# Kernel tuning notes

Hardware: AMD Instinct MI355X
Metric: run time of the kernel (lower is better)

The kernel has to match this reference:

```python
import jax, jax.numpy as jnp
import numpy as np

B, S, D = 2, 2048, 2048
H, KV, HD = 32, 8, 64          # n_heads, n_kv_heads, head_dim
REP = H // KV                  # 4
THETA = 10000.0


def _rotate_half(u):
    h = u.shape[-1] // 2
    return jnp.concatenate([-u[..., h:], u[..., :h]], axis=-1)


def setup_inputs() -> dict:
    key = jax.random.key(0)
    ks = jax.random.split(key, 5)
    x = jax.random.normal(ks[0], (B, S, D), dtype=jnp.float32)
    Wq = jax.random.normal(ks[1], (D, H * HD), dtype=jnp.float32) * 0.02
    Wk = jax.random.normal(ks[2], (D, KV * HD), dtype=jnp.float32) * 0.02
    Wv = jax.random.normal(ks[3], (D, KV * HD), dtype=jnp.float32) * 0.02
    Wo = jax.random.normal(ks[4], (H * HD, D), dtype=jnp.float32) * 0.02
    return {"x": x, "Wq": Wq, "Wk": Wk, "Wv": Wv, "Wo": Wo}


def reference(x, Wq, Wk, Wv, Wo):
    b, s, d = x.shape
    # QKV projections (nn.Linear, no bias)
    q = (x @ Wq).reshape(b, s, H, HD).transpose(0, 2, 1, 3)   # [B,H,S,HD]
    k = (x @ Wk).reshape(b, s, KV, HD).transpose(0, 2, 1, 3)  # [B,KV,S,HD]
    v = (x @ Wv).reshape(b, s, KV, HD).transpose(0, 2, 1, 3)  # [B,KV,S,HD]

    # RoPE (position_offset = 0)
    inv_freq = 1.0 / (THETA ** (jnp.arange(0, HD, 2, dtype=jnp.float32) / HD))
    freqs = jnp.outer(jnp.arange(s, dtype=jnp.float32), inv_freq)  # [S,HD/2]
    emb = jnp.concatenate([freqs, freqs], axis=-1)                  # [S,HD]
    cos, sin = jnp.cos(emb), jnp.sin(emb)
    q = q * cos + _rotate_half(q) * sin
    k = k * cos + _rotate_half(k) * sin

    # Grouped attention: avoid materializing repeated KV tensors.
    qg = q.reshape(b, KV, REP, s, HD)                               # [B,KV,REP,S,HD]
    scale = 1.0 / np.sqrt(HD)
    scores = jnp.einsum('bgrqd,bgkd->bgrqk', qg, k) * scale         # [B,KV,REP,S,S]
    causal = jnp.tril(jnp.ones((s, s), dtype=bool))
    scores = jnp.where(causal, scores, jnp.finfo(jnp.float32).min)
    probs = jax.nn.softmax(scores.astype(jnp.float32), axis=-1).astype(q.dtype)
    out = jnp.einsum('bgrqk,bgkd->bgrqd', probs, v)                 # [B,KV,REP,S,HD]
    out = out.reshape(b, H, s, HD).transpose(0, 2, 1, 3).reshape(b, s, H * HD)
    return out @ Wo                                                  # [B,S,D]
```

## Files before the change

### kernel.cpp

```cpp
#include <hip/hip_runtime.h>
#include <math.h>

typedef __bf16 bf16_t;
typedef bf16_t bf16x8 __attribute__((ext_vector_type(8)));
typedef bf16_t bf16x4 __attribute__((ext_vector_type(4)));
typedef float floatx4 __attribute__((ext_vector_type(4)));
typedef short short4v __attribute__((ext_vector_type(4)));

#define MFMA16(a, b, c) __builtin_amdgcn_mfma_f32_16x16x32_bf16((a), (b), (c), 0, 0, 0)

#if __has_builtin(__builtin_amdgcn_exp2f)
#define PEXP(x) __builtin_amdgcn_exp2f(x)
#define SCORE_SCALE (0.125f * 1.4426950408889634f)
#else
#define PEXP(x) __expf(x)
#define SCORE_SCALE 0.125f
#endif

#if __has_builtin(__builtin_amdgcn_mfma_f32_16x16x16bf16_1k)
#define HAVE_MFMA_K16 1
__device__ __forceinline__ floatx4 mfma_k16(bf16x4 a, bf16x4 b, floatx4 c)
{
    union { bf16x4 v; short4v s; } ua, ub;
    ua.v = a; ub.v = b;
    return __builtin_amdgcn_mfma_f32_16x16x16bf16_1k(ua.s, ub.s, c, 0, 0, 0);
}
#endif

union PU { unsigned u[2]; bf16x4 v; };
union BU { unsigned u[4]; bf16x8 v; };

__device__ __forceinline__ void gld16(const void* g, void* lds)
{
    __builtin_amdgcn_global_load_lds(
        reinterpret_cast<const __attribute__((address_space(1))) void*>(
            reinterpret_cast<uintptr_t>(g)),
        reinterpret_cast<__attribute__((address_space(3))) void*>(
            (unsigned int)reinterpret_cast<uintptr_t>(lds)),
        16, 0, 0);
}

template <int RND>
__device__ __forceinline__ void stageT(
    const bf16_t* __restrict__ g, int K, int r0, int k0,
    bf16_t* lds, int tid, int wave)
{
    #pragma unroll
    for (int i = 0; i < RND; ++i) {
        int c = i * 512 + tid, r = c >> 3, s = c & 7;
        gld16(g + (size_t)(r0 + r) * K + k0 + ((s ^ (r & 7)) << 3),
              lds + (size_t)(i * 512 + wave * 64) * 8);
    }
}

template <typename TC, int BN>
__device__ __forceinline__ void gemm256_body(
    const bf16_t* __restrict__ A, const bf16_t* __restrict__ Bt,
    TC* __restrict__ C, int row0, int col0, int N, int K, bf16_t* smem)
{
    constexpr int NT = BN / 64;
    constexpr int NH = NT / 2;
    constexpr int RB = BN / 64;

    const int tid  = threadIdx.x;
    const int wave = tid >> 6, lane = tid & 63;
    const int quad = lane >> 4, l16 = lane & 15;
    const int wm = (wave >> 2) * 128;
    const int wn = (wave & 3) * (BN / 4);

    bf16_t* As0 = smem;
    bf16_t* As1 = smem + 256 * 64;
    bf16_t* Bs0 = smem + 2 * 256 * 64;
    bf16_t* Bs1 = Bs0 + BN * 64;

    const int ntile = K >> 6;

    floatx4 acc[8][NT] = {};

    stageT<4>(A, K, row0, 0, As0, tid, wave);
    stageT<RB>(Bt, K, col0, 0, Bs0, tid, wave);
    stageT<4>(A, K, row0, 64, As1, tid, wave);

    #pragma unroll 1
    for (int u = 0; u < ntile; ++u) {
        const int d = u & 1;
        bf16_t* Asd = d ? As1 : As0;
        bf16_t* Bsd = d ? Bs1 : Bs0;

        if (u + 1 < ntile)
            __asm__ volatile("s_waitcnt vmcnt(4)" ::: "memory");
        else
            __asm__ volatile("s_waitcnt vmcnt(0)" ::: "memory");
        __builtin_amdgcn_s_barrier();
        __asm__ volatile("" ::: "memory");

        if (u + 1 < ntile)
            stageT<RB>(Bt, K, col0, (u + 1) << 6, d ? Bs0 : Bs1, tid, wave);

        bf16x8 af[8][2], bfr[NH][2];
        #pragma unroll
        for (int mt = 0; mt < 8; ++mt)
            #pragma unroll
            for (int kh = 0; kh < 2; ++kh) {
                int ar = wm + mt * 16 + l16;
                af[mt][kh] = *(const bf16x8*)&Asd[ar * 64 +
                    (((kh * 4 + quad) ^ (ar & 7)) << 3)];
            }
        #pragma unroll
        for (int j = 0; j < NH; ++j)
            #pragma unroll
            for (int kh = 0; kh < 2; ++kh) {
                int br = wn + j * 16 + l16;
                bfr[j][kh] = *(const bf16x8*)&Bsd[br * 64 +
                    (((kh * 4 + quad) ^ (br & 7)) << 3)];
            }

        __builtin_amdgcn_s_setprio(1);
        #pragma unroll
        for (int kh = 0; kh < 2; ++kh)
            #pragma unroll
            for (int mt = 0; mt < 8; ++mt)
                #pragma unroll
                for (int j = 0; j < NH; ++j)
                    acc[mt][j] = MFMA16(af[mt][kh], bfr[j][kh], acc[mt][j]);
        __builtin_amdgcn_s_setprio(0);

        __asm__ volatile("s_waitcnt lgkmcnt(0)" ::: "memory");
        __builtin_amdgcn_s_barrier();
        __asm__ volatile("" ::: "memory");

        if (u + 2 < ntile)
            stageT<4>(A, K, row0, (u + 2) << 6, Asd, tid, wave);

        bf16x8 bf1[NH][2];
        #pragma unroll
        for (int j = 0; j < NH; ++j)
            #pragma unroll
            for (int kh = 0; kh < 2; ++kh) {
                int br = wn + (NH + j) * 16 + l16;
                bf1[j][kh] = *(const bf16x8*)&Bsd[br * 64 +
                    (((kh * 4 + quad) ^ (br & 7)) << 3)];
            }

        __builtin_amdgcn_s_setprio(1);
        #pragma unroll
        for (int kh = 0; kh < 2; ++kh)
            #pragma unroll
            for (int mt = 0; mt < 8; ++mt)
                #pragma unroll
                for (int j = 0; j < NH; ++j)
                    acc[mt][NH + j] = MFMA16(af[mt][kh], bf1[j][kh],
                                             acc[mt][NH + j]);
        __builtin_amdgcn_s_setprio(0);
    }

    #pragma unroll
    for (int mt = 0; mt < 8; ++mt)
        #pragma unroll
        for (int nt = 0; nt < NT; ++nt)
            #pragma unroll
            for (int r = 0; r < 4; ++r)
                C[(size_t)(row0 + wm + mt * 16 + quad * 4 + r) * N
                  + col0 + wn + nt * 16 + l16] = (TC)acc[mt][nt][r];
}

__global__ __launch_bounds__(512, 2) void gemm256_qkv(
    const bf16_t* __restrict__ A, const bf16_t* __restrict__ BtQ,
    const bf16_t* __restrict__ BtK, const bf16_t* __restrict__ BtV,
    bf16_t* __restrict__ CQ, bf16_t* __restrict__ CK, bf16_t* __restrict__ CV)
{
    extern __shared__ __align__(16) bf16_t smem[];
    const int x = blockIdx.x;
    const bf16_t* Bt; bf16_t* C; int N, col0;
    if (x < 8)       { Bt = BtQ; C = CQ; N = 2048; col0 = x * 256; }
    else if (x < 10) { Bt = BtK; C = CK; N = 512;  col0 = (x - 8) * 256; }
    else             { Bt = BtV; C = CV; N = 512;  col0 = (x - 10) * 256; }
    gemm256_body<bf16_t, 256>(A, Bt, C, blockIdx.y * 256, col0, N, 2048, smem);
}

__global__ __launch_bounds__(512, 2) void gemm256_out(
    const bf16_t* __restrict__ A, const bf16_t* __restrict__ Bt,
    float* __restrict__ C)
{
    extern __shared__ __align__(16) bf16_t smem[];
    gemm256_body<float, 128>(A, Bt, C, blockIdx.y * 256, blockIdx.x * 128,
                             2048, 2048, smem);
}

__device__ __forceinline__ void transpose_body(
    const float* __restrict__ W, bf16_t* __restrict__ Wt, int K, int N,
    int bx, int by, float (*t)[33], int tid)
{
    int tx = tid & 31, ty = tid >> 5;
    #pragma unroll
    for (int i = 0; i < 32; i += 8)
        t[ty + i][tx] = W[(size_t)(by + ty + i) * N + bx + tx];
    __syncthreads();
    #pragma unroll
    for (int i = 0; i < 32; i += 8)
        Wt[(size_t)(bx + ty + i) * K + by + tx] = (bf16_t)t[tx][ty + i];
}

__global__ __launch_bounds__(256) void prep_all(
    const float* __restrict__ x, const float* __restrict__ Wq,
    const float* __restrict__ Wk, const float* __restrict__ Wv,
    bf16_t* __restrict__ xb, bf16_t* __restrict__ WqT,
    bf16_t* __restrict__ WkT, bf16_t* __restrict__ WvT)
{
    __shared__ float t[32][33];
    const int blk = blockIdx.x, tid = threadIdx.x;
    if (blk < 8192) {
        int i = blk * 256 + tid;
        float4 f = ((const float4*)x)[i];
        bf16x4 v = {(bf16_t)f.x, (bf16_t)f.y, (bf16_t)f.z, (bf16_t)f.w};
        ((bf16x4*)xb)[i] = v;
    } else if (blk < 12288) {
        int r = blk - 8192;
        transpose_body(Wq, WqT, 2048, 2048, (r & 63) * 32, (r >> 6) * 32, t, tid);
    } else if (blk < 13312) {
        int r = blk - 12288;
        transpose_body(Wk, WkT, 2048, 512, (r & 15) * 32, (r >> 4) * 32, t, tid);
    } else {
        int r = blk - 13312;
        transpose_body(Wv, WvT, 2048, 512, (r & 15) * 32, (r >> 4) * 32, t, tid);
    }
}

__global__ __launch_bounds__(256) void mid_all(
    bf16_t* __restrict__ Kw, const bf16_t* __restrict__ Vw,
    bf16_t* __restrict__ VtG, const float* __restrict__ Wo,
    bf16_t* __restrict__ WoT)
{
    __shared__ float tf[32][33];
    __shared__ bf16_t tb[32][34];
    const int blk = blockIdx.x, tid = threadIdx.x;
    if (blk < 4096) {
        int idx = blk * 256 + tid;
        int i   = idx & 31;
        int h   = (idx >> 5) & 7;
        int row = idx >> 8;
        int pos = row & 2047;
        float invf = powf(10000.0f, -(float)i / 32.0f);
        float sv, cv;
        sincosf((float)pos * invf, &sv, &cv);
        size_t base = (size_t)row * 512 + (size_t)h * 64 + i;
        float a  = (float)Kw[base];
        float b2 = (float)Kw[base + 32];
        Kw[base]      = (bf16_t)(a * cv - b2 * sv);
        Kw[base + 32] = (bf16_t)(b2 * cv + a * sv);
    } else if (blk < 6144) {
        int r  = blk - 4096;
        int bz = r >> 10, r2 = r & 1023;
        int bx = (r2 & 15) * 32, by = (r2 >> 4) * 32;
        int tx = tid & 31, ty = tid >> 5;
        #pragma unroll
        for (int i = 0; i < 32; i += 8)
            tb[ty + i][tx] = Vw[((size_t)bz * 2048 + by + ty + i) * 512 + bx + tx];
        __syncthreads();
        #pragma unroll
        for (int i = 0; i < 32; i += 8)
            VtG[((size_t)bz * 512 + bx + ty + i) * 2048 + by + tx] = tb[tx][ty + i];
    } else {
        int r = blk - 6144;
        transpose_body(Wo, WoT, 2048, 2048, (r & 63) * 32, (r >> 6) * 32, tf, tid);
    }
}

__global__ __launch_bounds__(256, 2) void gqa_attn(
    const bf16_t* __restrict__ Q, const bf16_t* __restrict__ Kc,
    const bf16_t* __restrict__ Vt, bf16_t* __restrict__ AO)
{
    __shared__ alignas(16) bf16_t Ks[2][128 * 64];
    __shared__ alignas(16) bf16_t Vs[2][128 * 64];

    const int bid = blockIdx.x;
    const int l   = (bid & 7) * 64 + (bid >> 3);
    const int g   = l >> 6;
    const int b   = (l >> 5) & 1;
    const int x   = l & 31;

    const int tid  = threadIdx.x;
    const int wave = tid >> 6, lane = tid & 63;
    const int quad = lane >> 4, l16 = lane & 15;
    const int h = g * 4 + wave;

    #pragma unroll 1
    for (int t = 0; t < 2; ++t) {
        const int qt = t ? x : (63 - x);
        const int q0 = qt * 32;
        int qb[2];
        qb[0] = q0;
        qb[1] = q0 + 16;

        bf16x8 qf[2][2];
        #pragma unroll
        for (int mt = 0; mt < 2; ++mt) {
            int qrow = qb[mt] + l16;
            const bf16_t* qp = Q + (size_t)(b * 2048 + qrow) * 2048 + h * 64 + quad * 8;
            bf16x8 lo = *(const bf16x8*)qp;
            bf16x8 hi = *(const bf16x8*)(qp + 32);
            #pragma unroll
            for (int j = 0; j < 8; ++j) {
                int d = quad * 8 + j;
                float invf = powf(10000.0f, -(float)d / 32.0f);
                float sv, cv;
                sincosf((float)qrow * invf, &sv, &cv);
                float a = (float)lo[j], c2 = (float)hi[j];
                qf[mt][0][j] = (bf16_t)((a * cv - c2 * sv) * SCORE_SCALE);
                qf[mt][1][j] = (bf16_t)((c2 * cv + a * sv) * SCORE_SCALE);
            }
        }

        floatx4 o[2][4] = {};
        floatx4 ls4[2] = {};

        const int ktmax = qt >> 1;
        const int nwin  = (ktmax >> 1) + 1;

        auto STAGE = [&](int win, int dst) {
            const int kbase = win * 128;
            #pragma unroll
            for (int i = 0; i < 4; ++i) {
                int c = i * 256 + tid, r = c >> 3, s = c & 7;
                int sw = (s ^ (r & 7)) << 3;
                gld16(Kc + (size_t)(b * 2048 + kbase + r) * 512 + g * 64 + sw,
                      &Ks[dst][(i * 256 + wave * 64) * 8]);
            }
            #pragma unroll
            for (int i = 0; i < 4; ++i) {
                int c = i * 256 + tid;
                int ci = c & 511, hw = c >> 9;
                int r = ci >> 3, s = ci & 7;
                int sw = (s ^ (r & 7)) << 3;
                gld16(Vt + (size_t)(b * 512 + g * 64 + r) * 2048
                         + kbase + hw * 64 + sw,
                      &Vs[dst][(i * 256 + wave * 64) * 8]);
            }
        };

        __asm__ volatile("s_waitcnt lgkmcnt(0)" ::: "memory");
        __builtin_amdgcn_s_barrier();
        STAGE(0, 0);

        #pragma unroll 1
        for (int win = 0; win < nwin; ++win) {
            const int cur = win & 1;
            if (win + 1 < nwin) {
                STAGE(win + 1, cur ^ 1);
                __asm__ volatile("s_waitcnt vmcnt(8)" ::: "memory");
            } else {
                __asm__ volatile("s_waitcnt vmcnt(0)" ::: "memory");
            }
            __builtin_amdgcn_s_barrier();

            #pragma unroll
            for (int hw = 0; hw < 2; ++hw) {
                const int kt = 2 * win + hw;
                if (kt <= ktmax) {
                    const bf16_t* Ksh = &Ks[cur][hw * 4096];
                    const bf16_t* Vsh = &Vs[cur][hw * 4096];

                    floatx4 st[2][4] = {};
                    __builtin_amdgcn_s_setprio(1);
                    #pragma unroll
                    for (int nt = 0; nt < 4; ++nt) {
                        int kr = nt * 16 + l16;
                        bf16x8 kf0 = *(const bf16x8*)&Ksh[kr * 64 + ((quad ^ (kr & 7)) << 3)];
                        bf16x8 kf1 = *(const bf16x8*)&Ksh[kr * 64 + (((4 + quad) ^ (kr & 7)) << 3)];
                        st[0][nt] = MFMA16(kf0, qf[0][0], st[0][nt]);
                        st[0][nt] = MFMA16(kf1, qf[0][1], st[0][nt]);
                        st[1][nt] = MFMA16(kf0, qf[1][0], st[1][nt]);
                        st[1][nt] = MFMA16(kf1, qf[1][1], st[1][nt]);
                    }
                    __builtin_amdgcn_s_setprio(0);

                    PU pk[2][4];
                    const bool diag = (kt == ktmax);
                    #pragma unroll
                    for (int mt = 0; mt < 2; ++mt) {
                        const int qa = qb[mt] + l16;
                        #pragma unroll
                        for (int nt = 0; nt < 4; ++nt) {
                            float pv[4];
                            #pragma unroll
                            for (int r = 0; r < 4; ++r) {
                                float e = PEXP(st[mt][nt][r]);
                                if (diag) {
                                    int ka = kt * 64 + nt * 16 + quad * 4 + r;
                                    if (ka > qa) e = 0.f;
                                }
                                ls4[mt][r] += e;
                                pv[r] = e;
                            }
                            pk[mt][nt].v = bf16x4{(bf16_t)pv[0], (bf16_t)pv[1],
                                                  (bf16_t)pv[2], (bf16_t)pv[3]};
                        }
                    }

#ifdef HAVE_MFMA_K16
                    __builtin_amdgcn_s_setprio(1);
                    #pragma unroll
                    for (int nt = 0; nt < 4; ++nt)
                        #pragma unroll
                        for (int dt = 0; dt < 4; ++dt) {
                            int vr = dt * 16 + l16;
                            int slot = ((nt << 1) | (quad >> 1)) ^ (vr & 7);
                            bf16x4 va = *(const bf16x4*)&Vsh[vr * 64 + (slot << 3)
                                                             + ((quad & 1) << 2)];
                            o[0][dt] = mfma_k16(va, pk[0][nt].v, o[0][dt]);
                            o[1][dt] = mfma_k16(va, pk[1][nt].v, o[1][dt]);
                        }
                    __builtin_amdgcn_s_setprio(0);
#else
                    #pragma unroll
                    for (int H = 0; H < 2; ++H) {
                        BU bfv[2];
                        #pragma unroll
                        for (int mt = 0; mt < 2; ++mt) {
                            #pragma unroll
                            for (int j = 0; j < 4; ++j) {
                                int srcl = (((quad & 1) << 1) + (j >> 1)) * 16 + l16;
                                unsigned a0 = (unsigned)__shfl((int)pk[mt][2 * H].u[j & 1], srcl, 64);
                                unsigned a1 = (unsigned)__shfl((int)pk[mt][2 * H + 1].u[j & 1], srcl, 64);
                                bfv[mt].u[j] = (quad >> 1) ? a1 : a0;
                            }
                        }
                        #pragma unroll
                        for (int dt = 0; dt < 4; ++dt) {
                            int vr = dt * 16 + l16;
                            bf16x8 va = *(const bf16x8*)&Vsh[vr * 64
                                          + ((((H << 2) | quad) ^ (vr & 7)) << 3)];
                            o[0][dt] = MFMA16(va, bfv[0].v, o[0][dt]);
                            o[1][dt] = MFMA16(va, bfv[1].v, o[1][dt]);
                        }
                    }
#endif
                }
            }

            __asm__ volatile("s_waitcnt lgkmcnt(0)" ::: "memory");
            __builtin_amdgcn_s_barrier();
        }

        #pragma unroll
        for (int mt = 0; mt < 2; ++mt) {
            float l2 = ls4[mt][0] + ls4[mt][1] + ls4[mt][2] + ls4[mt][3];
            l2 += __shfl_xor(l2, 16, 64);
            l2 += __shfl_xor(l2, 32, 64);
            float rc = 1.0f / l2;
            #pragma unroll
            for (int dt = 0; dt < 4; ++dt) {
                bf16x4 ov = {(bf16_t)(o[mt][dt][0] * rc), (bf16_t)(o[mt][dt][1] * rc),
                             (bf16_t)(o[mt][dt][2] * rc), (bf16_t)(o[mt][dt][3] * rc)};
                *(bf16x4*)&AO[(size_t)(b * 2048 + qb[mt] + l16) * 2048
                              + h * 64 + dt * 16 + quad * 4] = ov;
            }
        }
    }
}

extern "C" void kernel_launch(void* const* d_in, const int* in_sizes, int n_in,
                              void* d_out, int out_size, void* d_ws, size_t ws_size,
                              hipStream_t stream)
{
    const float* x  = (const float*)d_in[0];
    const float* Wq = (const float*)d_in[1];
    const float* Wk = (const float*)d_in[2];
    const float* Wv = (const float*)d_in[3];
    const float* Wo = (const float*)d_in[4];
    float* out = (float*)d_out;

    const size_t MB = 1024 * 1024;
    char* ws = (char*)d_ws;
    bf16_t* xb_AO = (bf16_t*)(ws);
    bf16_t* WqoT  = (bf16_t*)(ws + 16 * MB);
    bf16_t* WkT   = (bf16_t*)(ws + 24 * MB);
    bf16_t* WvT   = (bf16_t*)(ws + 26 * MB);
    bf16_t* Qw    = (bf16_t*)(ws + 28 * MB);
    bf16_t* Kw    = (bf16_t*)(ws + 44 * MB);
    bf16_t* Vw    = (bf16_t*)(ws + 48 * MB);
    bf16_t* VtG   = (bf16_t*)(ws + 52 * MB);

    static bool s_attr = false;
    if (!s_attr) {
        hipFuncSetAttribute(reinterpret_cast<const void*>(gemm256_qkv),
                            hipFuncAttributeMaxDynamicSharedMemorySize, 131072);
        hipFuncSetAttribute(reinterpret_cast<const void*>(gemm256_out),
                            hipFuncAttributeMaxDynamicSharedMemorySize, 98304);
        s_attr = true;
    }

    prep_all<<<14336, 256, 0, stream>>>(x, Wq, Wk, Wv, xb_AO, WqoT, WkT, WvT);

    gemm256_qkv<<<dim3(12, 16), 512, 131072, stream>>>(
        xb_AO, WqoT, WkT, WvT, Qw, Kw, Vw);

    mid_all<<<10240, 256, 0, stream>>>(Kw, Vw, VtG, Wo, WqoT);

    gqa_attn<<<dim3(512), 256, 0, stream>>>(Qw, Kw, VtG, xb_AO);

    gemm256_out<<<dim3(16, 16), 512, 98304, stream>>>(xb_AO, WqoT, out);
}
```

Measured before the change: 290.9 us.

## Restructure GEMM main loop into four-phase ping-pong schedule with split staging

Rewrites the shared 256-row GEMM body used by the QKV and output projections as a four-phase loop. Each phase reads a quarter of the A/B fragments from LDS, issues part of the next tile's global-to-LDS staging, then runs a barrier-bracketed MFMA block. The aim is finer interleaving of memory traffic and matrix math and lower register pressure by holding only half the A fragments at a time. In exchange each K-tile now has eight barriers instead of two and must re-read B fragments from LDS.

```diff
diff --git a/kernel.cpp b/kernel.cpp
--- a/kernel.cpp
+++ b/kernel.cpp
@@ -40,27 +40,32 @@
         16, 0, 0);
 }
 
-template <int RND>
-__device__ __forceinline__ void stageT(
-    const bf16_t* __restrict__ g, int K, int r0, int k0,
-    bf16_t* lds, int tid, int wave)
-{
-    #pragma unroll
-    for (int i = 0; i < RND; ++i) {
-        int c = i * 512 + tid, r = c >> 3, s = c & 7;
-        gld16(g + (size_t)(r0 + r) * K + k0 + ((s ^ (r & 7)) << 3),
-              lds + (size_t)(i * 512 + wave * 64) * 8);
-    }
+template <int N>
+__device__ __forceinline__ void vmw()
+{
+    __asm__ volatile("s_waitcnt vmcnt(%0)" :: "n"(N) : "memory");
+}
+
+__device__ __forceinline__ void barx()
+{
+    __asm__ volatile("" ::: "memory");
+    __builtin_amdgcn_s_barrier();
+    __asm__ volatile("" ::: "memory");
+}
+
+__device__ __forceinline__ void lgk0()
+{
+    __asm__ volatile("s_waitcnt lgkmcnt(0)" ::: "memory");
 }
 
 template <typename TC, int BN>
-__device__ __forceinline__ void gemm256_body(
+__device__ __forceinline__ void gemm_ph_body(
     const bf16_t* __restrict__ A, const bf16_t* __restrict__ Bt,
     TC* __restrict__ C, int row0, int col0, int N, int K, bf16_t* smem)
 {
-    constexpr int NT = BN / 64;
-    constexpr int NH = NT / 2;
-    constexpr int RB = BN / 64;
+    constexpr int NT  = BN / 64;
+    constexpr int NH  = NT / 2;
+    constexpr int RBH = BN / 128;
 
     const int tid  = threadIdx.x;
     const int wave = tid >> 6, lane = tid & 63;
@@ -76,83 +81,112 @@
     const int ntile = K >> 6;
 
     floatx4 acc[8][NT] = {};
-
-    stageT<4>(A, K, row0, 0, As0, tid, wave);
-    stageT<RB>(Bt, K, col0, 0, Bs0, tid, wave);
-    stageT<4>(A, K, row0, 64, As1, tid, wave);
+    bf16x8  af[4][2];
+    bf16x8  bfr[NH][2];
+    bf16x8  bf1[NH][2];
+
+#define PH_STG_A(Bf, h, uu) do {                                              \
+    _Pragma("unroll")                                                         \
+    for (int _i = 0; _i < 2; ++_i) {                                          \
+        int _c = _i * 512 + tid, _r = (h) * 128 + (_c >> 3), _s = _c & 7;     \
+        gld16(A + (size_t)(row0 + _r) * K + ((uu) << 6)                       \
+                + ((_s ^ (_r & 7)) << 3),                                     \
+              (Bf) + (h) * 8192 + (_i * 512 + wave * 64) * 8);                \
+    } } while (0)
+
+#define PH_STG_B(Bf, h, uu) do {                                              \
+    _Pragma("unroll")                                                         \
+    for (int _i = 0; _i < RBH; ++_i) {                                        \
+        int _c = _i * 512 + tid, _r = (h) * (BN / 2) + (_c >> 3), _s = _c & 7;\
+        gld16(Bt + (size_t)(col0 + _r) * K + ((uu) << 6)                      \
+                 + ((_s ^ (_r & 7)) << 3),                                    \
+              (Bf) + (h) * (BN / 2) * 64 + (_i * 512 + wave * 64) * 8);       \
+    } } while (0)
+
+#define PH_RD_A(MH) do {                                                      \
+    _Pragma("unroll")                                                         \
+    for (int _i = 0; _i < 4; ++_i)                                            \
+        _Pragma("unroll")                                                     \
+        for (int _kh = 0; _kh < 2; ++_kh) {                                   \
+            int _ar = wm + ((MH) * 4 + _i) * 16 + l16;                        \
+            af[_i][_kh] = *(const bf16x8*)&Asd[_ar * 64 +                     \
+                (((_kh * 4 + quad) ^ (_ar & 7)) << 3)];                       \
+        } } while (0)
+
+#define PH_RD_B(Reg, NF) do {                                                 \
+    _Pragma("unroll")                                                         \
+    for (int _j = 0; _j < NH; ++_j)                                           \
+        _Pragma("unroll")                                                     \
+        for (int _kh = 0; _kh < 2; ++_kh) {                                   \
+            int _br = wn + ((NF) * NH + _j) * 16 + l16;                       \
+            Reg[_j][_kh] = *(const bf16x8*)&Bsd[_br * 64 +                    \
+                (((_kh * 4 + quad) ^ (_br & 7)) << 3)];                       \
+        } } while (0)
+
+#define PH_MM(MB, Reg, NF) do {                                               \
+    __builtin_amdgcn_s_setprio(1);                                            \
+    _Pragma("unroll")                                                         \
+    for (int _kh = 0; _kh < 2; ++_kh)                                         \
+        _Pragma("unroll")                                                     \
+        for (int _i = 0; _i < 4; ++_i)                                        \
+            _Pragma("unroll")                                                 \
+            for (int _j = 0; _j < NH; ++_j)                                   \
+                acc[(MB) * 4 + _i][(NF) * NH + _j] =                          \
+                    MFMA16(af[_i][_kh], Reg[_j][_kh],                         \
+                           acc[(MB) * 4 + _i][(NF) * NH + _j]);               \
+    __builtin_amdgcn_s_setprio(0);                                            \
+} while (0)
+
+    PH_STG_A(As0, 0, 0); PH_STG_A(As0, 1, 0);
+    PH_STG_B(Bs0, 0, 0); PH_STG_B(Bs0, 1, 0);
+    PH_STG_A(As1, 0, 1); PH_STG_A(As1, 1, 1);
+    vmw<4>();
+    barx();
 
     #pragma unroll 1
     for (int u = 0; u < ntile; ++u) {
         const int d = u & 1;
         bf16_t* Asd = d ? As1 : As0;
         bf16_t* Bsd = d ? Bs1 : Bs0;
-
-        if (u + 1 < ntile)
-            __asm__ volatile("s_waitcnt vmcnt(4)" ::: "memory");
-        else
-            __asm__ volatile("s_waitcnt vmcnt(0)" ::: "memory");
-        __builtin_amdgcn_s_barrier();
-        __asm__ volatile("" ::: "memory");
-
-        if (u + 1 < ntile)
-            stageT<RB>(Bt, K, col0, (u + 1) << 6, d ? Bs0 : Bs1, tid, wave);
-
-        bf16x8 af[8][2], bfr[NH][2];
-        #pragma unroll
-        for (int mt = 0; mt < 8; ++mt)
-            #pragma unroll
-            for (int kh = 0; kh < 2; ++kh) {
-                int ar = wm + mt * 16 + l16;
-                af[mt][kh] = *(const bf16x8*)&Asd[ar * 64 +
-                    (((kh * 4 + quad) ^ (ar & 7)) << 3)];
-            }
-        #pragma unroll
-        for (int j = 0; j < NH; ++j)
-            #pragma unroll
-            for (int kh = 0; kh < 2; ++kh) {
-                int br = wn + j * 16 + l16;
-                bfr[j][kh] = *(const bf16x8*)&Bsd[br * 64 +
-                    (((kh * 4 + quad) ^ (br & 7)) << 3)];
-            }
-
-        __builtin_amdgcn_s_setprio(1);
-        #pragma unroll
-        for (int kh = 0; kh < 2; ++kh)
-            #pragma unroll
-            for (int mt = 0; mt < 8; ++mt)
-                #pragma unroll
-                for (int j = 0; j < NH; ++j)
-                    acc[mt][j] = MFMA16(af[mt][kh], bfr[j][kh], acc[mt][j]);
-        __builtin_amdgcn_s_setprio(0);
-
-        __asm__ volatile("s_waitcnt lgkmcnt(0)" ::: "memory");
-        __builtin_amdgcn_s_barrier();
-        __asm__ volatile("" ::: "memory");
-
-        if (u + 2 < ntile)
-            stageT<4>(A, K, row0, (u + 2) << 6, Asd, tid, wave);
-
-        bf16x8 bf1[NH][2];
-        #pragma unroll
-        for (int j = 0; j < NH; ++j)
-            #pragma unroll
-            for (int kh = 0; kh < 2; ++kh) {
-                int br = wn + (NH + j) * 16 + l16;
-                bf1[j][kh] = *(const bf16x8*)&Bsd[br * 64 +
-                    (((kh * 4 + quad) ^ (br & 7)) << 3)];
-            }
-
-        __builtin_amdgcn_s_setprio(1);
-        #pragma unroll
-        for (int kh = 0; kh < 2; ++kh)
-            #pragma unroll
-            for (int mt = 0; mt < 8; ++mt)
-                #pragma unroll
-                for (int j = 0; j < NH; ++j)
-                    acc[mt][NH + j] = MFMA16(af[mt][kh], bf1[j][kh],
-                                             acc[mt][NH + j]);
-        __builtin_amdgcn_s_setprio(0);
+        bf16_t* Bsn = d ? Bs0 : Bs1;
+        const bool nl1 = (u + 1 < ntile);
+        const bool nl2 = (u + 2 < ntile);
+
+        PH_RD_A(0);
+        PH_RD_B(bfr, 0);
+        if (nl1) PH_STG_B(Bsn, 0, u + 1);
+        barx(); lgk0();
+        PH_MM(0, bfr, 0);
+        barx();
+
+        PH_RD_B(bf1, 1);
+        if (nl1) PH_STG_B(Bsn, 1, u + 1);
+        barx(); lgk0();
+        PH_MM(0, bf1, 1);
+        barx();
+
+        PH_RD_A(1);
+        barx(); lgk0();
+        PH_MM(1, bf1, 1);
+        barx();
+
+        PH_RD_B(bfr, 0);
+        if (nl2) {
+            PH_STG_A(Asd, 0, u + 2); PH_STG_A(Asd, 1, u + 2);
+            vmw<4>();
+        } else {
+            vmw<0>();
+        }
+        barx(); lgk0();
+        PH_MM(1, bfr, 0);
+        barx();
     }
+
+#undef PH_STG_A
+#undef PH_STG_B
+#undef PH_RD_A
+#undef PH_RD_B
+#undef PH_MM
 
     #pragma unroll
     for (int mt = 0; mt < 8; ++mt)
@@ -175,7 +209,7 @@
     if (x < 8)       { Bt = BtQ; C = CQ; N = 2048; col0 = x * 256; }
     else if (x < 10) { Bt = BtK; C = CK; N = 512;  col0 = (x - 8) * 256; }
     else             { Bt = BtV; C = CV; N = 512;  col0 = (x - 10) * 256; }
-    gemm256_body<bf16_t, 256>(A, Bt, C, blockIdx.y * 256, col0, N, 2048, smem);
+    gemm_ph_body<bf16_t, 256>(A, Bt, C, blockIdx.y * 256, col0, N, 2048, smem);
 }
 
 __global__ __launch_bounds__(512, 2) void gemm256_out(
@@ -183,7 +217,7 @@
     float* __restrict__ C)
 {
     extern __shared__ __align__(16) bf16_t smem[];
-    gemm256_body<float, 128>(A, Bt, C, blockIdx.y * 256, blockIdx.x * 128,
+    gemm_ph_body<float, 128>(A, Bt, C, blockIdx.y * 256, blockIdx.x * 128,
                              2048, 2048, smem);
 }
 
```

Result: slower. 299.3 us (+2.9%).

## Replace 256-tile GEMMs with 128x128 tiles and simpler double-buffered pipeline

Applied to the files above, without the earlier changes.

Swaps the 256-row, 512-thread GEMM kernels for QKV and output projections with 128x128 tiles on 256 threads. The staggered A/B prefetch and split-N MFMA phases become a plain double buffer that loads the next A and B tiles at the top of each iteration. The grids grow to 768 and 512 blocks, which should fill the CUs better and lets each block use 64KB of LDS. In exchange, each element loaded is reused less, and global and LDS traffic per FLOP goes up.

```diff
diff --git a/kernel.cpp b/kernel.cpp
--- a/kernel.cpp
+++ b/kernel.cpp
@@ -40,46 +40,58 @@
         16, 0, 0);
 }
 
-template <int RND>
-__device__ __forceinline__ void stageT(
+template <int N>
+__device__ __forceinline__ void vmw()
+{
+    __asm__ volatile("s_waitcnt vmcnt(%0)" :: "n"(N) : "memory");
+}
+
+__device__ __forceinline__ void barx()
+{
+    __asm__ volatile("" ::: "memory");
+    __builtin_amdgcn_s_barrier();
+    __asm__ volatile("" ::: "memory");
+}
+
+__device__ __forceinline__ void lgk0()
+{
+    __asm__ volatile("s_waitcnt lgkmcnt(0)" ::: "memory");
+}
+
+__device__ __forceinline__ void stage128(
     const bf16_t* __restrict__ g, int K, int r0, int k0,
     bf16_t* lds, int tid, int wave)
 {
     #pragma unroll
-    for (int i = 0; i < RND; ++i) {
-        int c = i * 512 + tid, r = c >> 3, s = c & 7;
+    for (int i = 0; i < 4; ++i) {
+        int c = i * 256 + tid, r = c >> 3, s = c & 7;
         gld16(g + (size_t)(r0 + r) * K + k0 + ((s ^ (r & 7)) << 3),
-              lds + (size_t)(i * 512 + wave * 64) * 8);
-    }
-}
-
-template <typename TC, int BN>
-__device__ __forceinline__ void gemm256_body(
+              lds + (size_t)(i * 256 + wave * 64) * 8);
+    }
+}
+
+template <typename TC>
+__device__ __forceinline__ void gemm128_body(
     const bf16_t* __restrict__ A, const bf16_t* __restrict__ Bt,
     TC* __restrict__ C, int row0, int col0, int N, int K, bf16_t* smem)
 {
-    constexpr int NT = BN / 64;
-    constexpr int NH = NT / 2;
-    constexpr int RB = BN / 64;
-
     const int tid  = threadIdx.x;
     const int wave = tid >> 6, lane = tid & 63;
     const int quad = lane >> 4, l16 = lane & 15;
-    const int wm = (wave >> 2) * 128;
-    const int wn = (wave & 3) * (BN / 4);
+    const int wm = (wave >> 1) * 64;
+    const int wn = (wave & 1) * 64;
 
     bf16_t* As0 = smem;
-    bf16_t* As1 = smem + 256 * 64;
-    bf16_t* Bs0 = smem + 2 * 256 * 64;
-    bf16_t* Bs1 = Bs0 + BN * 64;
+    bf16_t* As1 = smem + 8192;
+    bf16_t* Bs0 = smem + 16384;
+    bf16_t* Bs1 = smem + 24576;
 
     const int ntile = K >> 6;
 
-    floatx4 acc[8][NT] = {};
-
-    stageT<4>(A, K, row0, 0, As0, tid, wave);
-    stageT<RB>(Bt, K, col0, 0, Bs0, tid, wave);
-    stageT<4>(A, K, row0, 64, As1, tid, wave);
+    floatx4 acc[4][4] = {};
+
+    stage128(A, K, row0, 0, As0, tid, wave);
+    stage128(Bt, K, col0, 0, Bs0, tid, wave);
 
     #pragma unroll 1
     for (int u = 0; u < ntile; ++u) {
@@ -87,19 +99,18 @@
         bf16_t* Asd = d ? As1 : As0;
         bf16_t* Bsd = d ? Bs1 : Bs0;
 
-        if (u + 1 < ntile)
-            __asm__ volatile("s_waitcnt vmcnt(4)" ::: "memory");
-        else
-            __asm__ volatile("s_waitcnt vmcnt(0)" ::: "memory");
-        __builtin_amdgcn_s_barrier();
-        __asm__ volatile("" ::: "memory");
-
-        if (u + 1 < ntile)
-            stageT<RB>(Bt, K, col0, (u + 1) << 6, d ? Bs0 : Bs1, tid, wave);
-
-        bf16x8 af[8][2], bfr[NH][2];
-        #pragma unroll
-        for (int mt = 0; mt < 8; ++mt)
+        if (u + 1 < ntile) {
+            stage128(A, K, row0, (u + 1) << 6, d ? As0 : As1, tid, wave);
+            stage128(Bt, K, col0, (u + 1) << 6, d ? Bs0 : Bs1, tid, wave);
+            vmw<8>();
+        } else {
+            vmw<0>();
+        }
+        barx();
+
+        bf16x8 af[4][2], bfr[4][2];
+        #pragma unroll
+        for (int mt = 0; mt < 4; ++mt)
             #pragma unroll
             for (int kh = 0; kh < 2; ++kh) {
                 int ar = wm + mt * 16 + l16;
@@ -107,11 +118,11 @@
                     (((kh * 4 + quad) ^ (ar & 7)) << 3)];
             }
         #pragma unroll
-        for (int j = 0; j < NH; ++j)
+        for (int nt = 0; nt < 4; ++nt)
             #pragma unroll
             for (int kh = 0; kh < 2; ++kh) {
-                int br = wn + j * 16 + l16;
-                bfr[j][kh] = *(const bf16x8*)&Bsd[br * 64 +
+                int br = wn + nt * 16 + l16;
+                bfr[nt][kh] = *(const bf16x8*)&Bsd[br * 64 +
                     (((kh * 4 + quad) ^ (br & 7)) << 3)];
             }
 
@@ -119,52 +130,27 @@
         #pragma unroll
         for (int kh = 0; kh < 2; ++kh)
             #pragma unroll
-            for (int mt = 0; mt < 8; ++mt)
+            for (int mt = 0; mt < 4; ++mt)
                 #pragma unroll
-                for (int j = 0; j < NH; ++j)
-                    acc[mt][j] = MFMA16(af[mt][kh], bfr[j][kh], acc[mt][j]);
+                for (int nt = 0; nt < 4; ++nt)
+                    acc[mt][nt] = MFMA16(af[mt][kh], bfr[nt][kh], acc[mt][nt]);
         __builtin_amdgcn_s_setprio(0);
 
-        __asm__ volatile("s_waitcnt lgkmcnt(0)" ::: "memory");
-        __builtin_amdgcn_s_barrier();
-        __asm__ volatile("" ::: "memory");
-
-        if (u + 2 < ntile)
-            stageT<4>(A, K, row0, (u + 2) << 6, Asd, tid, wave);
-
-        bf16x8 bf1[NH][2];
-        #pragma unroll
-        for (int j = 0; j < NH; ++j)
-            #pragma unroll
-            for (int kh = 0; kh < 2; ++kh) {
-                int br = wn + (NH + j) * 16 + l16;
-                bf1[j][kh] = *(const bf16x8*)&Bsd[br * 64 +
-                    (((kh * 4 + quad) ^ (br & 7)) << 3)];
-            }
-
-        __builtin_amdgcn_s_setprio(1);
-        #pragma unroll
-        for (int kh = 0; kh < 2; ++kh)
-            #pragma unroll
-            for (int mt = 0; mt < 8; ++mt)
-                #pragma unroll
-                for (int j = 0; j < NH; ++j)
-                    acc[mt][NH + j] = MFMA16(af[mt][kh], bf1[j][kh],
-                                             acc[mt][NH + j]);
-        __builtin_amdgcn_s_setprio(0);
+        lgk0();
+        barx();
     }
 
     #pragma unroll
-    for (int mt = 0; mt < 8; ++mt)
-        #pragma unroll
-        for (int nt = 0; nt < NT; ++nt)
+    for (int mt = 0; mt < 4; ++mt)
+        #pragma unroll
+        for (int nt = 0; nt < 4; ++nt)
             #pragma unroll
             for (int r = 0; r < 4; ++r)
                 C[(size_t)(row0 + wm + mt * 16 + quad * 4 + r) * N
                   + col0 + wn + nt * 16 + l16] = (TC)acc[mt][nt][r];
 }
 
-__global__ __launch_bounds__(512, 2) void gemm256_qkv(
+__global__ __launch_bounds__(256, 2) void gemm128_qkv(
     const bf16_t* __restrict__ A, const bf16_t* __restrict__ BtQ,
     const bf16_t* __restrict__ BtK, const bf16_t* __restrict__ BtV,
     bf16_t* __restrict__ CQ, bf16_t* __restrict__ CK, bf16_t* __restrict__ CV)
@@ -172,19 +158,19 @@
     extern __shared__ __align__(16) bf16_t smem[];
     const int x = blockIdx.x;
     const bf16_t* Bt; bf16_t* C; int N, col0;
-    if (x < 8)       { Bt = BtQ; C = CQ; N = 2048; col0 = x * 256; }
-    else if (x < 10) { Bt = BtK; C = CK; N = 512;  col0 = (x - 8) * 256; }
-    else             { Bt = BtV; C = CV; N = 512;  col0 = (x - 10) * 256; }
-    gemm256_body<bf16_t, 256>(A, Bt, C, blockIdx.y * 256, col0, N, 2048, smem);
-}
-
-__global__ __launch_bounds__(512, 2) void gemm256_out(
+    if (x < 16)      { Bt = BtQ; C = CQ; N = 2048; col0 = x * 128; }
+    else if (x < 20) { Bt = BtK; C = CK; N = 512;  col0 = (x - 16) * 128; }
+    else             { Bt = BtV; C = CV; N = 512;  col0 = (x - 20) * 128; }
+    gemm128_body<bf16_t>(A, Bt, C, blockIdx.y * 128, col0, N, 2048, smem);
+}
+
+__global__ __launch_bounds__(256, 2) void gemm128_out(
     const bf16_t* __restrict__ A, const bf16_t* __restrict__ Bt,
     float* __restrict__ C)
 {
     extern __shared__ __align__(16) bf16_t smem[];
-    gemm256_body<float, 128>(A, Bt, C, blockIdx.y * 256, blockIdx.x * 128,
-                             2048, 2048, smem);
+    gemm128_body<float>(A, Bt, C, blockIdx.y * 128, blockIdx.x * 128,
+                        2048, 2048, smem);
 }
 
 __device__ __forceinline__ void transpose_body(
@@ -483,21 +469,21 @@
 
     static bool s_attr = false;
     if (!s_attr) {
-        hipFuncSetAttribute(reinterpret_cast<const void*>(gemm256_qkv),
-                            hipFuncAttributeMaxDynamicSharedMemorySize, 131072);
-        hipFuncSetAttribute(reinterpret_cast<const void*>(gemm256_out),
-                            hipFuncAttributeMaxDynamicSharedMemorySize, 98304);
+        hipFuncSetAttribute(reinterpret_cast<const void*>(gemm128_qkv),
+                            hipFuncAttributeMaxDynamicSharedMemorySize, 65536);
+        hipFuncSetAttribute(reinterpret_cast<const void*>(gemm128_out),
+                            hipFuncAttributeMaxDynamicSharedMemorySize, 65536);
         s_attr = true;
     }
 
     prep_all<<<14336, 256, 0, stream>>>(x, Wq, Wk, Wv, xb_AO, WqoT, WkT, WvT);
 
-    gemm256_qkv<<<dim3(12, 16), 512, 131072, stream>>>(
+    gemm128_qkv<<<dim3(24, 32), 256, 65536, stream>>>(
         xb_AO, WqoT, WkT, WvT, Qw, Kw, Vw);
 
     mid_all<<<10240, 256, 0, stream>>>(Kw, Vw, VtG, Wo, WqoT);
 
     gqa_attn<<<dim3(512), 256, 0, stream>>>(Qw, Kw, VtG, xb_AO);
 
-    gemm256_out<<<dim3(16, 16), 512, 98304, stream>>>(xb_AO, WqoT, out);
-}
+    gemm128_out<<<dim3(16, 32), 256, 65536, stream>>>(xb_AO, WqoT, out);
+}
```

Result: no change. 288.1 us (-1.0%).
